# Performance work log

Measured on AMD Instinct MI355X. Metric: run time of the kernel, lower is better.

## Reference

```python
import jax, jax.numpy as jnp
import numpy as np

SELF_ATTN = -5e4  # reformer TOKEN_SELF_ATTN_VALUE


def _lsh_self_attention(h, w_qk, w_v, w_out, b_out, rotations, n_heads, bucket_size):
    # h: [B, N, D] with N divisible by 2*bucket_size (pre-padded)
    B, N, D = h.shape
    E = D // n_heads
    n_buckets = N // bucket_size
    n_hashes = rotations.shape[1]
    # shared-QK projections, heads merged into batch (batch-major, like reformer)
    qk = (h @ w_qk).reshape(B, N, n_heads, E).transpose(0, 2, 1, 3).reshape(B * n_heads, N, E)
    v = (h @ w_v).reshape(B, N, n_heads, E).transpose(0, 2, 1, 3).reshape(B * n_heads, N, E)
    # --- LSH hashing: argmax over [rot, -rot] ---
    rot = jnp.einsum('bne,ehr->bhnr', qk, rotations)          # [BH, n_hashes, N, n_buckets/2]
    rot = jnp.concatenate([rot, -rot], axis=-1)               # [BH, n_hashes, N, n_buckets]
    buckets = jnp.argmax(rot, axis=-1)                        # [BH, n_hashes, N]
    buckets = buckets + (jnp.arange(n_hashes) * n_buckets)[None, :, None]
    buckets = buckets.reshape(B * n_heads, n_hashes * N)
    # --- sort tokens by (bucket, position) ---
    ticker = jnp.arange(n_hashes * N)
    buckets_and_t = N * buckets + (ticker % N)                # unique keys -> deterministic sort
    sticker = jnp.argsort(buckets_and_t, axis=-1)
    undo = jnp.argsort(sticker, axis=-1)
    st = sticker % N                                          # original positions, sorted order
    sqk = jnp.take_along_axis(qk, st[..., None], axis=1)      # [BH, n_hashes*N, E]
    sv = jnp.take_along_axis(v, st[..., None], axis=1)
    # --- chunk and attend locally (with look-one-back) ---
    nc = n_hashes * n_buckets
    bq = sqk.reshape(-1, nc, bucket_size, E)
    bk = bq / jnp.maximum(jnp.linalg.norm(bq, axis=-1, keepdims=True), 1e-12)  # normalized shared keys
    bv = sv.reshape(-1, nc, bucket_size, E)
    bts = st.reshape(-1, nc, bucket_size)
    look = lambda t: jnp.concatenate([t, jnp.roll(t, 1, axis=1)], axis=2)
    bk, bv, bkt = look(bk), look(bv), look(bts)
    dots = jnp.einsum('bcie,bcje->bcij', bq, bk) * (E ** -0.5)  # [BH, nc, bs, 2*bs]
    dots = jnp.where(bts[..., :, None] == bkt[..., None, :], SELF_ATTN, dots)  # mask self
    lse = jax.scipy.special.logsumexp(dots, axis=-1, keepdims=True)
    p = jnp.exp(dots - lse)
    bo = jnp.einsum('bcij,bcje->bcie', p, bv)
    so = bo.reshape(-1, n_hashes * N, E)
    slog = lse.reshape(-1, n_hashes * N)
    # --- unsort and combine hash rounds by softmax over logsumexp logits ---
    o = jnp.take_along_axis(so, undo[..., None], axis=1).reshape(-1, n_hashes, N, E)
    logits = jnp.take_along_axis(slog, undo, axis=1).reshape(-1, n_hashes, N, 1)
    probs = jnp.exp(logits - jax.scipy.special.logsumexp(logits, axis=1, keepdims=True))
    out = jnp.sum(o * probs, axis=1)                          # [BH, N, E]
    out = out.reshape(B, n_heads, N, E).transpose(0, 2, 1, 3).reshape(B, N, D)
    return out @ w_out + b_out


def setup_inputs() -> dict:
    key = jax.random.key(0)
    ks = jax.random.split(key, 8)
    b, l, n = 16, 12, 325
    d_feat, d_pos, heads, bucket, n_hashes = 256, 64, 8, 16, 4
    pad = 2 * bucket - n % (2 * bucket)
    n_buckets = (n + pad) // bucket
    E = d_feat // heads
    s = 0.05
    return {
        'x': jax.random.normal(ks[0], (b, l, n, d_feat), dtype=jnp.float32),
        'ste': jax.random.normal(ks[1], (b, l, n, d_pos), dtype=jnp.float32),
        'w_proj': jax.random.normal(ks[2], (d_feat + d_pos, d_feat), dtype=jnp.float32) * s,
        'b_proj': jnp.zeros((d_feat,), jnp.float32),
        'w_qk': jax.random.normal(ks[3], (d_feat, d_feat), dtype=jnp.float32) * s,
        'w_v': jax.random.normal(ks[4], (d_feat, d_feat), dtype=jnp.float32) * s,
        'w_out': jax.random.normal(ks[5], (d_feat, d_feat), dtype=jnp.float32) * s,
        'b_out': jnp.zeros((d_feat,), jnp.float32),
        'rotations': jax.random.normal(ks[6], (E, n_hashes, n_buckets // 2), dtype=jnp.float32),
        'n_heads': heads,
        'bucket_size': bucket,
    }


def reference(x, ste, w_proj, b_proj, w_qk, w_v, w_out, b_out, rotations, n_heads, bucket_size):
    b, l, n, d = x.shape
    h = jnp.concatenate([x, ste], axis=-1).reshape(b * l, n, -1)
    h = h @ w_proj + b_proj                                   # projection to d_hidden_feat
    pad = 2 * bucket_size - n % (2 * bucket_size)             # always > 0 (as in the source)
    h = jnp.pad(h, ((0, 0), (0, pad), (0, 0)))
    h = _lsh_self_attention(h, w_qk, w_v, w_out, b_out, rotations, n_heads, bucket_size)
    h = h[:, :-pad, :]
    return h.reshape(b, l, n, -1)
```

## Files before the change

### kernel.cpp

```cpp
#include <hip/hip_runtime.h>
#include <math.h>

#define BL 192
#define NREAL 325
#define NPAD 352
#define DM 256
#define DPOS 64
#define DIN 320
#define NHEADS 8
#define EDIM 32
#define NHASH 4
#define BS 16
#define NBUCK 22
#define NCHUNK 88
#define BHTOT 1536
#define RROT 11
#define W2COLS 352
#define RTM 8
#define HTM 16
#define QKP 9

__global__ __launch_bounds__(256) void h_kernel(
    const float* __restrict__ x, const float* __restrict__ ste,
    const float* __restrict__ wproj, const float* __restrict__ bproj,
    float* __restrict__ h) {
  int tile = blockIdx.x, bl = blockIdx.y;
  int d = threadIdx.x;
  int n0 = tile * HTM;
  float acc[HTM];
#pragma unroll
  for (int m = 0; m < HTM; ++m) acc[m] = 0.f;
  if (n0 + HTM <= NREAL) {
    const float* xb = x + (size_t)(bl * NREAL + n0) * DM;
    const float* sb = ste + (size_t)(bl * NREAL + n0) * DPOS;
    for (int k = 0; k < DM; k += 4) {
      float b0 = wproj[(k + 0) * DM + d];
      float b1 = wproj[(k + 1) * DM + d];
      float b2 = wproj[(k + 2) * DM + d];
      float b3 = wproj[(k + 3) * DM + d];
#pragma unroll
      for (int m = 0; m < HTM; ++m) {
        const float* xr = xb + (size_t)m * DM + k;
        acc[m] = fmaf(xr[0], b0, acc[m]);
        acc[m] = fmaf(xr[1], b1, acc[m]);
        acc[m] = fmaf(xr[2], b2, acc[m]);
        acc[m] = fmaf(xr[3], b3, acc[m]);
      }
    }
    for (int k = 0; k < DPOS; k += 4) {
      float b0 = wproj[(DM + k + 0) * DM + d];
      float b1 = wproj[(DM + k + 1) * DM + d];
      float b2 = wproj[(DM + k + 2) * DM + d];
      float b3 = wproj[(DM + k + 3) * DM + d];
#pragma unroll
      for (int m = 0; m < HTM; ++m) {
        const float* sr = sb + (size_t)m * DPOS + k;
        acc[m] = fmaf(sr[0], b0, acc[m]);
        acc[m] = fmaf(sr[1], b1, acc[m]);
        acc[m] = fmaf(sr[2], b2, acc[m]);
        acc[m] = fmaf(sr[3], b3, acc[m]);
      }
    }
  } else if (n0 < NREAL) {
#pragma unroll
    for (int m = 0; m < HTM; ++m) {
      if (n0 + m < NREAL) {
        const float* xr = x + (size_t)(bl * NREAL + n0 + m) * DM;
        const float* sr = ste + (size_t)(bl * NREAL + n0 + m) * DPOS;
        for (int k = 0; k < DM; ++k) acc[m] = fmaf(xr[k], wproj[k * DM + d], acc[m]);
        for (int k = 0; k < DPOS; ++k)
          acc[m] = fmaf(sr[k], wproj[(DM + k) * DM + d], acc[m]);
      }
    }
  }
  float bb = bproj[d];
#pragma unroll
  for (int m = 0; m < HTM; ++m) {
    int n = n0 + m;
    h[((size_t)(bl * NPAD + n)) * DM + d] = (n < NREAL) ? (acc[m] + bb) : 0.f;
  }
}

__global__ __launch_bounds__(256) void qkv_rot_bucket_kernel(
    const float* __restrict__ h, const float* __restrict__ wqk,
    const float* __restrict__ wv, const float* __restrict__ rotations,
    int* __restrict__ buckets, float* __restrict__ qk_out,
    float* __restrict__ v_out) {
  int tile = blockIdx.x, bl = blockIdx.y;
  int tid = threadIdx.x;
  __shared__ float Qs[RTM][DM];
  __shared__ float Rs[RTM][W2COLS];
  int n0 = tile * RTM;
  const float* hb = h + (size_t)(bl * NPAD + n0) * DM;
  float aq[RTM], av[RTM];
#pragma unroll
  for (int m = 0; m < RTM; ++m) { aq[m] = 0.f; av[m] = 0.f; }
  for (int k = 0; k < DM; k += 4) {
    float q0 = wqk[(k + 0) * DM + tid];
    float q1 = wqk[(k + 1) * DM + tid];
    float q2 = wqk[(k + 2) * DM + tid];
    float q3 = wqk[(k + 3) * DM + tid];
    float w0 = wv[(k + 0) * DM + tid];
    float w1 = wv[(k + 1) * DM + tid];
    float w2 = wv[(k + 2) * DM + tid];
    float w3 = wv[(k + 3) * DM + tid];
#pragma unroll
    for (int m = 0; m < RTM; ++m) {
      const float* hr = hb + (size_t)m * DM + k;
      float a0 = hr[0], a1 = hr[1], a2 = hr[2], a3 = hr[3];
      aq[m] = fmaf(a0, q0, aq[m]);
      aq[m] = fmaf(a1, q1, aq[m]);
      aq[m] = fmaf(a2, q2, aq[m]);
      aq[m] = fmaf(a3, q3, aq[m]);
      av[m] = fmaf(a0, w0, av[m]);
      av[m] = fmaf(a1, w1, av[m]);
      av[m] = fmaf(a2, w2, av[m]);
      av[m] = fmaf(a3, w3, av[m]);
    }
  }
  {
    int head = tid >> 5, e = tid & 31;
    size_t bh = (size_t)(bl * NHEADS + head);
#pragma unroll
    for (int m = 0; m < RTM; ++m) {
      Qs[m][tid] = aq[m];
      int n = n0 + m;
      qk_out[(bh * NPAD + n) * EDIM + e] = aq[m];
      v_out[(bh * NPAD + n) * EDIM + e] = av[m];
    }
  }
  __syncthreads();
  for (int col = tid; col < W2COLS; col += 256) {
    int head = col / 44;
    int hr = col - head * 44;
    int hs = hr / RROT;
    int r = hr - hs * RROT;
    float acc[RTM];
#pragma unroll
    for (int m = 0; m < RTM; ++m) acc[m] = 0.f;
    {
#pragma clang fp contract(off)
      for (int e = 0; e < EDIM; ++e) {
        float rr = rotations[(e * NHASH + hs) * RROT + r];
#pragma unroll
        for (int m = 0; m < RTM; ++m) {
          float p = Qs[m][head * EDIM + e] * rr;
          acc[m] = acc[m] + p;
        }
      }
    }
#pragma unroll
    for (int m = 0; m < RTM; ++m) Rs[m][col] = acc[m];
  }
  __syncthreads();
  {
    int m = tid >> 5;
    int rest = tid & 31;
    int head = rest >> 2;
    int hs = rest & 3;
    int cbase = head * 44 + hs * RROT;
    float bestv = Rs[m][cbase];
    int best = 0;
    for (int r = 1; r < RROT; ++r) {
      float dv = Rs[m][cbase + r];
      if (dv > bestv) { bestv = dv; best = r; }
    }
    for (int r = 0; r < RROT; ++r) {
      float dv = -Rs[m][cbase + r];
      if (dv > bestv) { bestv = dv; best = RROT + r; }
    }
    int n = n0 + m;
    int bh = bl * NHEADS + head;
    buckets[((size_t)(bh * NHASH + hs)) * NPAD + n] = best;
  }
}

__global__ __launch_bounds__(384) void sort_kernel(const int* __restrict__ buckets,
                                                   int* __restrict__ st) {
  int bh = blockIdx.x, hs = blockIdx.y;
  int n = threadIdx.x;
  __shared__ int buck[NPAD];
  const int* brow = buckets + ((size_t)(bh * NHASH + hs)) * NPAD;
  if (n < NPAD) buck[n] = brow[n];
  __syncthreads();
  if (n < NPAD) {
    int b = buck[n];
    int dest = 0;
    for (int m2 = 0; m2 < NPAD; ++m2) {
      int bm = buck[m2];
      dest += (int)((bm < b) | ((bm == b) & (m2 < n)));
    }
    st[((size_t)(bh * NHASH + hs)) * NPAD + dest] = n;
  }
}

__global__ __launch_bounds__(512) void attn_fused_kernel(
    const float* __restrict__ qk, const float* __restrict__ v,
    const int* __restrict__ st, float* __restrict__ att) {
  int bh = blockIdx.x;
  int t = threadIdx.x;
  int w = t >> 6;
  int lane = t & 63;
  int i2 = lane >> 5;
  int j = lane & 31;

  __shared__ float4 qk4[NPAD][QKP];
  __shared__ int stf[NHASH * NPAD];
  __shared__ float ll_s[NHASH][NPAD];
  __shared__ float rnorm_s[NPAD];
  __shared__ float L_s[NPAD];

  const float* qkb = qk + (size_t)bh * NPAD * EDIM;
  const float* vb = v + (size_t)bh * NPAD * EDIM;
  const int* strow = st + (size_t)bh * (NHASH * NPAD);

  for (int idx = t; idx < NPAD * 8; idx += 512) {
    int n = idx >> 3, c4 = idx & 7;
    qk4[n][c4] = ((const float4*)qkb)[idx];
  }
  for (int idx = t; idx < NHASH * NPAD; idx += 512) stf[idx] = strow[idx];
  __syncthreads();
  for (int n = t; n < NPAD; n += 512) {
    const float* row = (const float*)qk4[n];
    float s = 0.f;
    for (int e = 0; e < EDIM; ++e) s = fmaf(row[e], row[e], s);
    rnorm_s[n] = 1.0f / fmaxf(sqrtf(s), 1e-12f);
  }
  __syncthreads();

  for (int c = w; c < NCHUNK; c += 8) {
    int pc = (c + NCHUNK - 1) % NCHUNK;
    int hs = c / NBUCK;
    int kp = (j < BS) ? stf[c * BS + j] : stf[pc * BS + (j - BS)];
    float kr[EDIM];
    {
      const float4* krow = qk4[kp];
#pragma unroll
      for (int e4 = 0; e4 < 8; ++e4) {
        float4 kv = krow[e4];
        kr[e4 * 4 + 0] = kv.x; kr[e4 * 4 + 1] = kv.y;
        kr[e4 * 4 + 2] = kv.z; kr[e4 * 4 + 3] = kv.w;
      }
    }
    float scale = rnorm_s[kp] * 0.17677669529663688f;
#pragma unroll
    for (int i = 0; i < 8; ++i) {
      int q = i * 2 + i2;
      int qp = stf[c * BS + q];
      const float4* qrow = qk4[qp];
      float dot = 0.f;
#pragma unroll
      for (int e4 = 0; e4 < 8; ++e4) {
        float4 qv = qrow[e4];
        dot = fmaf(qv.x, kr[e4 * 4 + 0], dot);
        dot = fmaf(qv.y, kr[e4 * 4 + 1], dot);
        dot = fmaf(qv.z, kr[e4 * 4 + 2], dot);
        dot = fmaf(qv.w, kr[e4 * 4 + 3], dot);
      }
      dot *= scale;
      if (qp == kp) dot = -50000.0f;
      float mx = dot;
#pragma unroll
      for (int off = 16; off > 0; off >>= 1) mx = fmaxf(mx, __shfl_xor(mx, off, 32));
      float ex = expf(dot - mx);
      float sm = ex;
#pragma unroll
      for (int off = 16; off > 0; off >>= 1) sm += __shfl_xor(sm, off, 32);
      if (j == 0) ll_s[hs][qp] = mx + logf(sm);
    }
  }
  __syncthreads();
  for (int n = t; n < NPAD; n += 512) {
    float l0 = ll_s[0][n], l1 = ll_s[1][n], l2 = ll_s[2][n], l3 = ll_s[3][n];
    float m = fmaxf(fmaxf(l0, l1), fmaxf(l2, l3));
    float s = expf(l0 - m) + expf(l1 - m) + expf(l2 - m) + expf(l3 - m);
    L_s[n] = m + logf(s);
  }
  __syncthreads();

  int head = bh & 7, bl = bh >> 3;
  float* attb = att + ((size_t)bl * NPAD) * DM + head * EDIM;
  for (int c = w; c < NCHUNK; c += 8) {
    int pc = (c + NCHUNK - 1) % NCHUNK;
    int kp = (j < BS) ? stf[c * BS + j] : stf[pc * BS + (j - BS)];
    float kr[EDIM];
    {
      const float4* krow = qk4[kp];
#pragma unroll
      for (int e4 = 0; e4 < 8; ++e4) {
        float4 kv = krow[e4];
        kr[e4 * 4 + 0] = kv.x; kr[e4 * 4 + 1] = kv.y;
        kr[e4 * 4 + 2] = kv.z; kr[e4 * 4 + 3] = kv.w;
      }
    }
    float scale = rnorm_s[kp] * 0.17677669529663688f;
    float vr[32];
#pragma unroll
    for (int jj = 0; jj < 32; ++jj) {
      int kpj = (jj < BS) ? stf[c * BS + jj] : stf[pc * BS + (jj - BS)];
      vr[jj] = vb[kpj * EDIM + j];
    }
#pragma unroll
    for (int i = 0; i < 8; ++i) {
      int q = i * 2 + i2;
      int qp = stf[c * BS + q];
      const float4* qrow = qk4[qp];
      float dot = 0.f;
#pragma unroll
      for (int e4 = 0; e4 < 8; ++e4) {
        float4 qv = qrow[e4];
        dot = fmaf(qv.x, kr[e4 * 4 + 0], dot);
        dot = fmaf(qv.y, kr[e4 * 4 + 1], dot);
        dot = fmaf(qv.z, kr[e4 * 4 + 2], dot);
        dot = fmaf(qv.w, kr[e4 * 4 + 3], dot);
      }
      dot *= scale;
      if (qp == kp) dot = -50000.0f;
      float p = expf(dot - L_s[qp]);
      float acc = 0.f;
#pragma unroll
      for (int jj = 0; jj < 32; ++jj) {
        float pb = __shfl(p, jj, 32);
        acc = fmaf(pb, vr[jj], acc);
      }
      atomicAdd(&attb[(size_t)qp * DM + j], acc);
    }
  }
}

__global__ __launch_bounds__(256) void outproj_kernel(
    const float* __restrict__ att, const float* __restrict__ w,
    const float* __restrict__ bias, float* __restrict__ out) {
  int tile = blockIdx.x, bl = blockIdx.y;
  int d = threadIdx.x;
  int n0 = tile * HTM;
  float acc[HTM];
#pragma unroll
  for (int m = 0; m < HTM; ++m) acc[m] = 0.f;
  if (n0 + HTM <= NREAL) {
    const float* ab = att + (size_t)(bl * NPAD + n0) * DM;
    for (int k = 0; k < DM; k += 4) {
      float b0 = w[(k + 0) * DM + d];
      float b1 = w[(k + 1) * DM + d];
      float b2 = w[(k + 2) * DM + d];
      float b3 = w[(k + 3) * DM + d];
#pragma unroll
      for (int m = 0; m < HTM; ++m) {
        const float* ar = ab + (size_t)m * DM + k;
        acc[m] = fmaf(ar[0], b0, acc[m]);
        acc[m] = fmaf(ar[1], b1, acc[m]);
        acc[m] = fmaf(ar[2], b2, acc[m]);
        acc[m] = fmaf(ar[3], b3, acc[m]);
      }
    }
  } else if (n0 < NREAL) {
#pragma unroll
    for (int m = 0; m < HTM; ++m) {
      if (n0 + m < NREAL) {
        const float* ar = att + (size_t)(bl * NPAD + n0 + m) * DM;
        for (int k = 0; k < DM; ++k) acc[m] = fmaf(ar[k], w[k * DM + d], acc[m]);
      }
    }
  } else {
    return;
  }
  float bb = bias[d];
#pragma unroll
  for (int m = 0; m < HTM; ++m) {
    int n = n0 + m;
    if (n < NREAL) out[((size_t)(bl * NREAL + n)) * DM + d] = acc[m] + bb;
  }
}

extern "C" void kernel_launch(void* const* d_in, const int* in_sizes, int n_in,
                              void* d_out, int out_size, void* d_ws, size_t ws_size,
                              hipStream_t stream) {
  (void)in_sizes; (void)n_in; (void)out_size;
  const float* x = (const float*)d_in[0];
  const float* ste = (const float*)d_in[1];
  const float* w_proj = (const float*)d_in[2];
  const float* b_proj = (const float*)d_in[3];
  const float* w_qk = (const float*)d_in[4];
  const float* w_v = (const float*)d_in[5];
  const float* w_out = (const float*)d_in[6];
  const float* b_out = (const float*)d_in[7];
  const float* rotations = (const float*)d_in[8];
  float* out = (float*)d_out;

  const size_t szh = (size_t)BL * NPAD * DM;
  const size_t szst = (size_t)BHTOT * NHASH * NPAD;
  const size_t needed = 3 * szh * 4 + 2 * szst * 4;
  if (ws_size < needed) return;

  float* qk = (float*)d_ws;
  float* v = qk + szh;
  float* att = v + szh;
  float* h = att;
  int* st = (int*)(att + szh);
  int* buckets = st + szst;

  h_kernel<<<dim3(NPAD / HTM, BL), dim3(256), 0, stream>>>(
      x, ste, w_proj, b_proj, h);
  qkv_rot_bucket_kernel<<<dim3(NPAD / RTM, BL), dim3(256), 0, stream>>>(
      h, w_qk, w_v, rotations, buckets, qk, v);
  (void)hipMemsetAsync(att, 0, szh * sizeof(float), stream);
  sort_kernel<<<dim3(BHTOT, NHASH), dim3(384), 0, stream>>>(buckets, st);
  attn_fused_kernel<<<dim3(BHTOT), dim3(512), 0, stream>>>(qk, v, st, att);
  outproj_kernel<<<dim3(21, BL), dim3(256), 0, stream>>>(att, w_out, b_out, out);
}
```

Measured before the change: 1.671 ms.

## Swizzle shared QK layout, use 16-bit sort indices, broadcast queries via shuffles

The padded float4 shared array for QK rows is replaced with an XOR-swizzled layout, removing the padding and avoiding bank conflicts on row reads. The sorted-index table is stored as 16-bit values to shrink shared memory, and launch bounds request 4 blocks per SM so occupancy can rise. Query vectors are now loaded one element per lane and broadcast with 32 shuffles instead of 8 float4 shared loads per dot product. This trades shared-memory traffic for cross-lane shuffle work and possible register pressure from the tighter occupancy bound.

```diff
diff --git a/kernel.cpp b/kernel.cpp
--- a/kernel.cpp
+++ b/kernel.cpp
@@ -18,7 +18,6 @@
 #define W2COLS 352
 #define RTM 8
 #define HTM 16
-#define QKP 9
 
 __global__ __launch_bounds__(256) void h_kernel(
     const float* __restrict__ x, const float* __restrict__ ste,
@@ -194,7 +193,7 @@
   }
 }
 
-__global__ __launch_bounds__(512) void attn_fused_kernel(
+__global__ __launch_bounds__(512, 4) void attn_fused_kernel(
     const float* __restrict__ qk, const float* __restrict__ v,
     const int* __restrict__ st, float* __restrict__ att) {
   int bh = blockIdx.x;
@@ -204,8 +203,8 @@
   int i2 = lane >> 5;
   int j = lane & 31;
 
-  __shared__ float4 qk4[NPAD][QKP];
-  __shared__ int stf[NHASH * NPAD];
+  __shared__ float qk_s[NPAD * EDIM];
+  __shared__ unsigned short stf[NHASH * NPAD];
   __shared__ float ll_s[NHASH][NPAD];
   __shared__ float rnorm_s[NPAD];
   __shared__ float L_s[NPAD];
@@ -214,16 +213,22 @@
   const float* vb = v + (size_t)bh * NPAD * EDIM;
   const int* strow = st + (size_t)bh * (NHASH * NPAD);
 
+  float4* qk4 = (float4*)qk_s;
   for (int idx = t; idx < NPAD * 8; idx += 512) {
     int n = idx >> 3, c4 = idx & 7;
-    qk4[n][c4] = ((const float4*)qkb)[idx];
-  }
-  for (int idx = t; idx < NHASH * NPAD; idx += 512) stf[idx] = strow[idx];
+    qk4[(n * 8 + c4) ^ (n & 7)] = ((const float4*)qkb)[idx];
+  }
+  for (int idx = t; idx < NHASH * NPAD; idx += 512)
+    stf[idx] = (unsigned short)strow[idx];
   __syncthreads();
   for (int n = t; n < NPAD; n += 512) {
-    const float* row = (const float*)qk4[n];
+    int base = n * EDIM;
+    int sw = (n & 7) << 2;
     float s = 0.f;
-    for (int e = 0; e < EDIM; ++e) s = fmaf(row[e], row[e], s);
+    for (int e = 0; e < EDIM; ++e) {
+      float kv = qk_s[(base + e) ^ sw];
+      s = fmaf(kv, kv, s);
+    }
     rnorm_s[n] = 1.0f / fmaxf(sqrtf(s), 1e-12f);
   }
   __syncthreads();
@@ -234,10 +239,11 @@
     int kp = (j < BS) ? stf[c * BS + j] : stf[pc * BS + (j - BS)];
     float kr[EDIM];
     {
-      const float4* krow = qk4[kp];
+      const float4* krow4 = qk4;
+      int kb = kp * 8, ks = kp & 7;
 #pragma unroll
       for (int e4 = 0; e4 < 8; ++e4) {
-        float4 kv = krow[e4];
+        float4 kv = krow4[(kb + e4) ^ ks];
         kr[e4 * 4 + 0] = kv.x; kr[e4 * 4 + 1] = kv.y;
         kr[e4 * 4 + 2] = kv.z; kr[e4 * 4 + 3] = kv.w;
       }
@@ -247,15 +253,12 @@
     for (int i = 0; i < 8; ++i) {
       int q = i * 2 + i2;
       int qp = stf[c * BS + q];
-      const float4* qrow = qk4[qp];
+      float qreg = qk_s[(qp * EDIM + j) ^ ((qp & 7) << 2)];
       float dot = 0.f;
 #pragma unroll
-      for (int e4 = 0; e4 < 8; ++e4) {
-        float4 qv = qrow[e4];
-        dot = fmaf(qv.x, kr[e4 * 4 + 0], dot);
-        dot = fmaf(qv.y, kr[e4 * 4 + 1], dot);
-        dot = fmaf(qv.z, kr[e4 * 4 + 2], dot);
-        dot = fmaf(qv.w, kr[e4 * 4 + 3], dot);
+      for (int e = 0; e < EDIM; ++e) {
+        float qe = __shfl(qreg, e, 32);
+        dot = fmaf(qe, kr[e], dot);
       }
       dot *= scale;
       if (qp == kp) dot = -50000.0f;
@@ -285,10 +288,11 @@
     int kp = (j < BS) ? stf[c * BS + j] : stf[pc * BS + (j - BS)];
     float kr[EDIM];
     {
-      const float4* krow = qk4[kp];
+      const float4* krow4 = qk4;
+      int kb = kp * 8, ks = kp & 7;
 #pragma unroll
       for (int e4 = 0; e4 < 8; ++e4) {
-        float4 kv = krow[e4];
+        float4 kv = krow4[(kb + e4) ^ ks];
         kr[e4 * 4 + 0] = kv.x; kr[e4 * 4 + 1] = kv.y;
         kr[e4 * 4 + 2] = kv.z; kr[e4 * 4 + 3] = kv.w;
       }
@@ -304,15 +308,12 @@
     for (int i = 0; i < 8; ++i) {
       int q = i * 2 + i2;
       int qp = stf[c * BS + q];
-      const float4* qrow = qk4[qp];
+      float qreg = qk_s[(qp * EDIM + j) ^ ((qp & 7) << 2)];
       float dot = 0.f;
 #pragma unroll
-      for (int e4 = 0; e4 < 8; ++e4) {
-        float4 qv = qrow[e4];
-        dot = fmaf(qv.x, kr[e4 * 4 + 0], dot);
-        dot = fmaf(qv.y, kr[e4 * 4 + 1], dot);
-        dot = fmaf(qv.z, kr[e4 * 4 + 2], dot);
-        dot = fmaf(qv.w, kr[e4 * 4 + 3], dot);
+      for (int e = 0; e < EDIM; ++e) {
+        float qe = __shfl(qreg, e, 32);
+        dot = fmaf(qe, kr[e], dot);
       }
       dot *= scale;
       if (qp == kp) dot = -50000.0f;
```

Result: slower. 2.151 ms (+28.7%).
